# Optimization experiments

Hardware: AMD Instinct MI355X
Metric: run time of the kernel (lower is better)

## Reference

```python
import jax, jax.numpy as jnp
import numpy as np

B, CQ, CKV, H, W = 8, 128, 64, 64, 64
DIM = CQ // 8  # qk_reduction=8 -> 16


def conv1x1(x, w, b):
    # x: [B, Cin, H, W], w: [Cout, Cin], b: [Cout]
    return jnp.einsum('bchw,oc->bohw', x, w) + b[None, :, None, None]


def setup_inputs() -> dict:
    key = jax.random.key(0)
    ks = jax.random.split(key, 12)
    s = 0.05
    return {
        'x4q': jax.random.normal(ks[0], (B, CQ, H, W), jnp.float32),
        'x4kv': jax.random.normal(ks[1], (B, CKV, H, W), jnp.float32),
        'Wq': jax.random.normal(ks[2], (DIM, CQ), jnp.float32) * s,
        'bq': jax.random.normal(ks[3], (DIM,), jnp.float32) * s,
        'Wk': jax.random.normal(ks[4], (DIM, CKV), jnp.float32) * s,
        'bk': jax.random.normal(ks[5], (DIM,), jnp.float32) * s,
        'Wv': jax.random.normal(ks[6], (CQ, CKV), jnp.float32) * s,
        'bv': jax.random.normal(ks[7], (CQ,), jnp.float32) * s,
        'Wo': jax.random.normal(ks[8], (CQ, CQ), jnp.float32) * s,
        'bo': jax.random.normal(ks[9], (CQ,), jnp.float32) * s,
        'gamma': jax.random.normal(ks[10], (1,), jnp.float32) * s,
    }


def reference(x4q, x4kv, Wq, bq, Wk, bk, Wv, bv, Wo, bo, gamma):
    q = conv1x1(x4q, Wq, bq)    # [B, DIM, H, W]
    k = conv1x1(x4kv, Wk, bk)   # [B, DIM, H, W]
    v = conv1x1(x4kv, Wv, bv)   # [B, CQ,  H, W]
    b, dim, h_, w_ = q.shape
    n = h_ * w_
    qf = q.reshape(b, dim, n)
    kf = k.reshape(b, dim, n)
    vf = v.reshape(b, -1, n)
    # score[b, n_query, m_key] = q^T k, scaled by dim^-0.5
    score = jnp.einsum('bdn,bdm->bnm', qf, kf) * (float(dim) ** -0.5)
    attention = jax.nn.softmax(score, axis=2)          # over keys m
    hmat = jnp.einsum('bcm,bnm->bcn', vf, attention)   # bmm(v, att^T)
    hmap = hmat.reshape(b, -1, h_, w_)
    hmap = conv1x1(hmap, Wo, bo)
    return gamma * hmap + x4q
```

## Files before the change

### kernel.cpp

```cpp
#include <hip/hip_runtime.h>

#define NB 8
#define CQ 128
#define CKV 64
#define NPIX 4096
#define QDIM 16
#define KVBLK 128
#define NTI (NPIX / KVBLK)

typedef float f32x4 __attribute__((ext_vector_type(4)));
typedef float f32x16 __attribute__((ext_vector_type(16)));
typedef __bf16 bf16x8 __attribute__((ext_vector_type(8)));
typedef unsigned short u16;
typedef u16 u16x4 __attribute__((ext_vector_type(4)));
typedef u16 u16x8 __attribute__((ext_vector_type(8)));
typedef unsigned int u32;
typedef u32 u32x2 __attribute__((ext_vector_type(2)));
typedef u32 u32x4 __attribute__((ext_vector_type(4)));

static __device__ __forceinline__ u16 f2bf(float f) {
  unsigned int u = __builtin_bit_cast(unsigned int, f);
  u = (u + 0x7FFFu + ((u >> 16) & 1u)) >> 16;
  return (u16)u;
}
static __device__ __forceinline__ u32 cvtpk(float lo, float hi) {
  u32 r; asm("v_cvt_pk_bf16_f32 %0, %1, %2" : "=v"(r) : "v"(lo), "v"(hi)); return r;
}
static __device__ __forceinline__ void plswap(u32& a, u32& b) {
#if __has_builtin(__builtin_amdgcn_permlane32_swap)
  u32x2 r = __builtin_amdgcn_permlane32_swap(a, b, false, false);
  a = r[0]; b = r[1];
#else
  asm volatile("v_permlane32_swap_b32 %0, %1" : "+v"(a), "+v"(b));
#endif
}
static __device__ __forceinline__ void gload_lds16(const void* g, void* l) {
  __builtin_amdgcn_global_load_lds((const __attribute__((address_space(1))) void*)g,
                                   (__attribute__((address_space(3))) void*)l, 16, 0, 0);
}

__global__ __launch_bounds__(256) void proj_qk(
    const float* __restrict__ xq, const float* __restrict__ Wq, const float* __restrict__ bq,
    const float* __restrict__ xkv, const float* __restrict__ Wk, const float* __restrict__ bk,
    u16* __restrict__ Qs, u16* __restrict__ Ks)
{
  __shared__ float wq[QDIM][CQ];
  __shared__ float wk[QDIM][CKV];
  __shared__ float redq[4][64][17];
  __shared__ float redk[4][64][17];
  int t = threadIdx.x;
  for (int i = t; i < QDIM * CQ; i += 256) wq[i >> 7][i & 127] = Wq[i];
  for (int i = t; i < QDIM * CKV; i += 256) wk[i >> 6][i & 63] = Wk[i];
  __syncthreads();
  int b = (int)blockIdx.x >> 6;
  int n0 = ((int)blockIdx.x & 63) << 6;
  int px = t & 63, cg = t >> 6;
  int n = n0 + px;
  const float* xqp = xq + (size_t)b * CQ * NPIX + n;
  const float* xkp = xkv + (size_t)b * CKV * NPIX + n;
  float qa[QDIM], ka[QDIM];
  #pragma unroll
  for (int d = 0; d < QDIM; d++) { qa[d] = 0.f; ka[d] = 0.f; }
  int cq0 = cg * 32, ck0 = cg * 16;
  #pragma unroll 4
  for (int c = cq0; c < cq0 + 32; c++) {
    float x = xqp[(size_t)c * NPIX];
    #pragma unroll
    for (int d = 0; d < QDIM; d++) qa[d] = fmaf(wq[d][c], x, qa[d]);
  }
  #pragma unroll 4
  for (int c = ck0; c < ck0 + 16; c++) {
    float x = xkp[(size_t)c * NPIX];
    #pragma unroll
    for (int d = 0; d < QDIM; d++) ka[d] = fmaf(wk[d][c], x, ka[d]);
  }
  #pragma unroll
  for (int d = 0; d < QDIM; d++) { redq[cg][px][d] = qa[d]; redk[cg][px][d] = ka[d]; }
  __syncthreads();
  const float SC = 0.25f * 1.44269504088896340736f;
  int d0 = cg * 4;
  u16x4 oq, ok;
  #pragma unroll
  for (int j = 0; j < 4; j++) {
    float sq = redq[0][px][d0 + j] + redq[1][px][d0 + j]
             + redq[2][px][d0 + j] + redq[3][px][d0 + j] + bq[d0 + j];
    oq[j] = f2bf(sq * SC);
    float sk = redk[0][px][d0 + j] + redk[1][px][d0 + j]
             + redk[2][px][d0 + j] + redk[3][px][d0 + j] + bk[d0 + j];
    ok[j] = f2bf(sk);
  }
  size_t o = ((size_t)b * NPIX + n) * QDIM + d0;
  *(u16x4*)(Qs + o) = oq;
  *(u16x4*)(Ks + o) = ok;
}

__global__ __launch_bounds__(256) void proj_v(
    const float* __restrict__ xkv, const float* __restrict__ Wv, const float* __restrict__ bv,
    u16* __restrict__ Vt)
{
  __shared__ float wv[CQ][CKV + 1];
  __shared__ float xs[CKV][64 + 4];
  int t = threadIdx.x;
  int b = (int)blockIdx.x >> 6;
  int n0 = ((int)blockIdx.x & 63) << 6;
  for (int i = t; i < CQ * CKV; i += 256) wv[i >> 6][i & 63] = Wv[i];
  const float* xp = xkv + (size_t)b * CKV * NPIX + n0;
  for (int i = t; i < CKV * 16; i += 256) {
    int c = i >> 4, c4 = (i & 15) * 4;
    *(f32x4*)(&xs[c][c4]) = *(const f32x4*)(xp + (size_t)c * NPIX + c4);
  }
  __syncthreads();
  int cog = t >> 4, pg = t & 15;
  int co0 = cog * 8, p0 = pg * 4;
  float acc[8][4];
  #pragma unroll
  for (int j = 0; j < 8; j++) {
    float bb = bv[co0 + j];
    #pragma unroll
    for (int p = 0; p < 4; p++) acc[j][p] = bb;
  }
  #pragma unroll 2
  for (int c = 0; c < CKV; c++) {
    float xv[4];
    #pragma unroll
    for (int p = 0; p < 4; p++) xv[p] = xs[c][p0 + p];
    #pragma unroll
    for (int j = 0; j < 8; j++) {
      float wvv = wv[co0 + j][c];
      #pragma unroll
      for (int p = 0; p < 4; p++) acc[j][p] = fmaf(wvv, xv[p], acc[j][p]);
    }
  }
  #pragma unroll
  for (int j = 0; j < 8; j++) {
    u16x4 ov;
    #pragma unroll
    for (int p = 0; p < 4; p++) ov[p] = f2bf(acc[j][p]);
    *(u16x4*)(Vt + ((size_t)b * CQ + co0 + j) * NPIX + n0 + p0) = ov;
  }
}

__global__ __launch_bounds__(256, 2) void attn(
    const u16* __restrict__ Qs, const u16* __restrict__ Ks, const u16* __restrict__ Vt,
    u16* __restrict__ O)
{
  __shared__ u16 v_s[2][128][128];
  __shared__ float d_red[2][2][32];
  __shared__ float d_inv[2][32];

  int t = (int)threadIdx.x;
  int w = t >> 6, l = t & 63, l31 = l & 31, hi = l >> 5;
  int ph = w;
  int sw = ((int)blockIdx.x & 7) * 64 + ((int)blockIdx.x >> 3);
  int b = sw >> 6, q0 = (sw & 63) * 64;

  const u16* Qb = Qs + (size_t)b * NPIX * QDIM;
  const u16* Kb = Ks + (size_t)b * NPIX * QDIM;
  const u16* Vb = Vt + (size_t)b * CQ * NPIX;

  bf16x8 qf0 = *(const bf16x8*)(Qb + (size_t)(q0 + l31) * QDIM + hi * 8);
  bf16x8 qf1 = *(const bf16x8*)(Qb + (size_t)(q0 + 32 + l31) * QDIM + hi * 8);

  int row0 = w * 32 + (l >> 4);
  int lx = (l & 15) ^ (l >> 4);
  const u16* kp = Kb + (size_t)(ph * 32 + l31) * QDIM + hi * 8;
  int rsw = l31 & 15;

  f32x16 acc0[4], acc1[4];
  #pragma unroll
  for (int cb = 0; cb < 4; cb++)
    #pragma unroll
    for (int r = 0; r < 16; r++) { acc0[cb][r] = 0.f; acc1[cb][r] = 0.f; }
  float lsum0 = 0.f, lsum1 = 0.f;

  u32x4 afw0[2], afw1[2];

  auto PACK = [&](const f32x16& s, u32x4* aw, float& ls) {
    float pv[16];
    #pragma unroll
    for (int r = 0; r < 16; r++) {
      pv[r] = __builtin_amdgcn_exp2f(s[r]);
      ls += pv[r];
    }
    u32 a0 = cvtpk(pv[0], pv[1]),  b0 = cvtpk(pv[2], pv[3]);
    u32 c0 = cvtpk(pv[4], pv[5]),  d0 = cvtpk(pv[6], pv[7]);
    plswap(a0, c0); plswap(b0, d0);
    aw[0] = u32x4{a0, b0, c0, d0};
    u32 a1 = cvtpk(pv[8], pv[9]),  b1 = cvtpk(pv[10], pv[11]);
    u32 c1 = cvtpk(pv[12], pv[13]), d1 = cvtpk(pv[14], pv[15]);
    plswap(a1, c1); plswap(b1, d1);
    aw[1] = u32x4{a1, b1, c1, d1};
  };

  f32x16 z;
  #pragma unroll
  for (int r = 0; r < 16; r++) z[r] = 0.f;

  #pragma unroll
  for (int j = 0; j < 8; j++)
    gload_lds16(Vb + (size_t)(row0 + j * 4) * NPIX + (lx ^ ((j & 3) << 2)) * 8,
                &v_s[0][w * 32 + j * 4][0]);
  bf16x8 kc = *(const bf16x8*)(kp);
  bf16x8 kn = *(const bf16x8*)(kp + (size_t)KVBLK * QDIM);

  #pragma unroll 1
  for (int it = 0; it < NTI; it++) {
    __syncthreads();

    if (it + 1 < NTI) {
      #pragma unroll
      for (int j = 0; j < 8; j++)
        gload_lds16(Vb + (size_t)(row0 + j * 4) * NPIX + (lx ^ ((j & 3) << 2)) * 8
                       + (size_t)(it + 1) * KVBLK,
                    &v_s[(it + 1) & 1][w * 32 + j * 4][0]);
    }

    f32x16 s0 = __builtin_amdgcn_mfma_f32_32x32x16_bf16(kc, qf0, z, 0, 0, 0);
    f32x16 s1 = __builtin_amdgcn_mfma_f32_32x32x16_bf16(kc, qf1, z, 0, 0, 0);
    kc = kn;
    if (it + 2 < NTI) kn = *(const bf16x8*)(kp + (size_t)(it + 2) * KVBLK * QDIM);
    PACK(s0, afw0, lsum0);
    PACK(s1, afw1, lsum1);

    const u16 (*vs)[128] = v_s[it & 1];
    #pragma unroll
    for (int c = 0; c < 2; c++) {
      bf16x8 af0 = __builtin_bit_cast(bf16x8, afw0[c]);
      bf16x8 af1 = __builtin_bit_cast(bf16x8, afw1[c]);
      #pragma unroll
      for (int cb = 0; cb < 4; cb++) {
        int chunk = (ph * 4 + c * 2 + hi) ^ rsw;
        bf16x8 vf = *(const bf16x8*)(&vs[cb * 32 + l31][chunk * 8]);
        acc0[cb] = __builtin_amdgcn_mfma_f32_32x32x16_bf16(af0, vf, acc0[cb], 0, 0, 0);
        acc1[cb] = __builtin_amdgcn_mfma_f32_32x32x16_bf16(af1, vf, acc1[cb], 0, 0, 0);
      }
    }
  }

  float tot0 = lsum0 + __shfl_xor(lsum0, 32);
  float tot1 = lsum1 + __shfl_xor(lsum1, 32);
  __syncthreads();
  float* red = (float*)v_s;
  if (ph >= 2) {
    if (hi == 0) { d_red[ph - 2][0][l31] = tot0; d_red[ph - 2][1][l31] = tot1; }
    float* dst = red + (size_t)(ph - 2) * 64 * 128;
    #pragma unroll
    for (int cb = 0; cb < 4; cb++)
      #pragma unroll
      for (int r = 0; r < 16; r++) {
        int row = (r & 3) + 8 * (r >> 2) + 4 * hi;
        dst[(size_t)row * 128 + cb * 32 + l31] = acc0[cb][r];
        dst[(size_t)(row + 32) * 128 + cb * 32 + l31] = acc1[cb][r];
      }
  }
  __syncthreads();
  if (ph < 2) {
    tot0 += d_red[ph][0][l31];
    tot1 += d_red[ph][1][l31];
    const float* src = red + (size_t)ph * 64 * 128;
    #pragma unroll
    for (int cb = 0; cb < 4; cb++)
      #pragma unroll
      for (int r = 0; r < 16; r++) {
        int row = (r & 3) + 8 * (r >> 2) + 4 * hi;
        acc0[cb][r] += src[(size_t)row * 128 + cb * 32 + l31];
        acc1[cb][r] += src[(size_t)(row + 32) * 128 + cb * 32 + l31];
      }
  }
  __syncthreads();
  if (ph == 1) {
    if (hi == 0) { d_red[0][0][l31] = tot0; d_red[0][1][l31] = tot1; }
    float* dst = red;
    #pragma unroll
    for (int cb = 0; cb < 4; cb++)
      #pragma unroll
      for (int r = 0; r < 16; r++) {
        int row = (r & 3) + 8 * (r >> 2) + 4 * hi;
        dst[(size_t)row * 128 + cb * 32 + l31] = acc0[cb][r];
        dst[(size_t)(row + 32) * 128 + cb * 32 + l31] = acc1[cb][r];
      }
  }
  __syncthreads();
  if (ph == 0) {
    tot0 += d_red[0][0][l31];
    tot1 += d_red[0][1][l31];
    if (hi == 0) { d_inv[0][l31] = 1.0f / tot0; d_inv[1][l31] = 1.0f / tot1; }
    const float* src = red;
    u16* Ob = O + ((size_t)b * NPIX + q0) * CQ;
    #pragma unroll
    for (int cb = 0; cb < 4; cb++)
      #pragma unroll
      for (int r = 0; r < 16; r++) {
        int row = (r & 3) + 8 * (r >> 2) + 4 * hi;
        float v0 = acc0[cb][r] + src[(size_t)row * 128 + cb * 32 + l31];
        float v1 = acc1[cb][r] + src[(size_t)(row + 32) * 128 + cb * 32 + l31];
        Ob[(size_t)row * CQ + cb * 32 + l31] = f2bf(v0 * d_inv[0][row]);
        Ob[(size_t)(row + 32) * CQ + cb * 32 + l31] = f2bf(v1 * d_inv[1][row]);
      }
  }
}

__global__ __launch_bounds__(256) void proj_o(
    const u16* __restrict__ O, const float* __restrict__ Wo, const float* __restrict__ bo,
    const float* __restrict__ gamma, const float* __restrict__ xq, float* __restrict__ out)
{
  __shared__ u16 wo_s[128][136];
  __shared__ float bos[128];
  int t = (int)threadIdx.x, w = t >> 6, l = t & 63, l31 = l & 31, hi = l >> 5;
  int bb = (int)blockIdx.x >> 6;
  int n0 = ((int)blockIdx.x & 63) * 64;
  for (int i = t; i < 128 * 32; i += 256) {
    int r = i >> 5, c4 = (i & 31) * 4;
    f32x4 v = *(const f32x4*)(Wo + r * 128 + c4);
    #pragma unroll
    for (int j = 0; j < 4; j++) wo_s[r][c4 + j] = f2bf(v[j]);
  }
  if (t < 128) bos[t] = bo[t];
  __syncthreads();
  int nw = n0 + (w & 1) * 32;
  int coh = (w >> 1) * 64;
  const u16* Ob = O + ((size_t)bb * NPIX + nw) * CQ;
  f32x16 acc[2];
  #pragma unroll
  for (int cb = 0; cb < 2; cb++)
    #pragma unroll
    for (int r = 0; r < 16; r++) acc[cb][r] = 0.f;
  #pragma unroll
  for (int c = 0; c < 8; c++) {
    bf16x8 of = *(const bf16x8*)(Ob + (size_t)l31 * CQ + c * 16 + hi * 8);
    #pragma unroll
    for (int cb = 0; cb < 2; cb++) {
      bf16x8 wf = *(const bf16x8*)(&wo_s[coh + cb * 32 + l31][c * 16 + hi * 8]);
      acc[cb] = __builtin_amdgcn_mfma_f32_32x32x16_bf16(wf, of, acc[cb], 0, 0, 0);
    }
  }
  float g = gamma[0];
  #pragma unroll
  for (int cb = 0; cb < 2; cb++) {
    #pragma unroll
    for (int r = 0; r < 16; r++) {
      int co = coh + cb * 32 + (r & 3) + 8 * (r >> 2) + 4 * hi;
      size_t idx = ((size_t)bb * CQ + co) * NPIX + nw + l31;
      out[idx] = g * (acc[cb][r] + bos[co]) + xq[idx];
    }
  }
}

extern "C" void kernel_launch(void* const* d_in, const int* in_sizes, int n_in,
                              void* d_out, int out_size, void* d_ws, size_t ws_size,
                              hipStream_t stream) {
  const float* x4q  = (const float*)d_in[0];
  const float* x4kv = (const float*)d_in[1];
  const float* Wq   = (const float*)d_in[2];
  const float* bq   = (const float*)d_in[3];
  const float* Wk   = (const float*)d_in[4];
  const float* bk   = (const float*)d_in[5];
  const float* Wv   = (const float*)d_in[6];
  const float* bv   = (const float*)d_in[7];
  const float* Wo   = (const float*)d_in[8];
  const float* bo   = (const float*)d_in[9];
  const float* gamma = (const float*)d_in[10];
  float* out = (float*)d_out;

  u16* Qs = (u16*)d_ws;
  u16* Ks = Qs + (size_t)NB * NPIX * QDIM;
  u16* Vt = Ks + (size_t)NB * NPIX * QDIM;
  u16* O  = Vt + (size_t)NB * CQ * NPIX;

  proj_qk<<<dim3(NB * 64), dim3(256), 0, stream>>>(x4q, Wq, bq, x4kv, Wk, bk, Qs, Ks);
  proj_v<<<dim3(NB * 64), dim3(256), 0, stream>>>(x4kv, Wv, bv, Vt);
  attn<<<dim3(NB * 64), dim3(256), 0, stream>>>(Qs, Ks, Vt, O);
  proj_o<<<dim3(NB * 64), dim3(256), 0, stream>>>(O, Wo, bo, gamma, x4q, out);
}
```

Measured before the change: 86.11 us.

## Fuse output projection and residual epilogue into attention kernel

Removes the separate proj_o kernel. After the softmax-weighted V accumulation, the attention block normalises its 64-query tile, writes it as bf16 into a swizzled LDS buffer, and multiplies by Wo fragments held in registers using MFMA. It then adds bias, applies gamma and the residual, and writes the final output directly. It also restructures the cross-wave reduction so two waves each finish half the rows, instead of funnelling everything into wave 0. This avoids the global round-trip of the intermediate O tensor and one launch, at the cost of extra registers (woF), per-block Wo reloads, and a longer epilogue inside a kernel with occupancy 2.

```diff
diff --git a/kernel.cpp b/kernel.cpp
--- a/kernel.cpp
+++ b/kernel.cpp
@@ -142,11 +142,15 @@
 
 __global__ __launch_bounds__(256, 2) void attn(
     const u16* __restrict__ Qs, const u16* __restrict__ Ks, const u16* __restrict__ Vt,
-    u16* __restrict__ O)
+    const float* __restrict__ Wo, const float* __restrict__ bo,
+    const float* __restrict__ gamma, const float* __restrict__ xq,
+    float* __restrict__ out)
 {
   __shared__ u16 v_s[2][128][128];
   __shared__ float d_red[2][2][32];
+  __shared__ float d_x[2][32];
   __shared__ float d_inv[2][32];
+  __shared__ float bos[128];
 
   int t = (int)threadIdx.x;
   int w = t >> 6, l = t & 63, l31 = l & 31, hi = l >> 5;
@@ -157,6 +161,8 @@
   const u16* Qb = Qs + (size_t)b * NPIX * QDIM;
   const u16* Kb = Ks + (size_t)b * NPIX * QDIM;
   const u16* Vb = Vt + (size_t)b * CQ * NPIX;
+
+  if (t < 128) bos[t] = bo[t];
 
   bf16x8 qf0 = *(const bf16x8*)(Qb + (size_t)(q0 + l31) * QDIM + hi * 8);
   bf16x8 qf1 = *(const bf16x8*)(Qb + (size_t)(q0 + 32 + l31) * QDIM + hi * 8);
@@ -239,6 +245,20 @@
 
   float tot0 = lsum0 + __shfl_xor(lsum0, 32);
   float tot1 = lsum1 + __shfl_xor(lsum1, 32);
+
+  bf16x8 woF[8];
+  {
+    const float* wrow = Wo + (size_t)(w * 32 + l31) * CQ + hi * 8;
+    #pragma unroll
+    for (int kc8 = 0; kc8 < 8; kc8++) {
+      f32x4 a = *(const f32x4*)(wrow + kc8 * 16);
+      f32x4 c4 = *(const f32x4*)(wrow + kc8 * 16 + 4);
+      u32x4 pk = { cvtpk(a[0], a[1]), cvtpk(a[2], a[3]),
+                   cvtpk(c4[0], c4[1]), cvtpk(c4[2], c4[3]) };
+      woF[kc8] = __builtin_bit_cast(bf16x8, pk);
+    }
+  }
+
   __syncthreads();
   float* red = (float*)v_s;
   if (ph >= 2) {
@@ -266,82 +286,90 @@
         acc0[cb][r] += src[(size_t)row * 128 + cb * 32 + l31];
         acc1[cb][r] += src[(size_t)(row + 32) * 128 + cb * 32 + l31];
       }
-  }
-  __syncthreads();
-  if (ph == 1) {
-    if (hi == 0) { d_red[0][0][l31] = tot0; d_red[0][1][l31] = tot1; }
-    float* dst = red;
+    if (ph == 0) {
+      if (hi == 0) d_x[0][l31] = tot1;
+      #pragma unroll
+      for (int cb = 0; cb < 4; cb++)
+        #pragma unroll
+        for (int r = 0; r < 16; r++) {
+          int row = (r & 3) + 8 * (r >> 2) + 4 * hi;
+          red[(size_t)(row + 32) * 128 + cb * 32 + l31] = acc1[cb][r];
+        }
+    } else {
+      if (hi == 0) d_x[1][l31] = tot0;
+      #pragma unroll
+      for (int cb = 0; cb < 4; cb++)
+        #pragma unroll
+        for (int r = 0; r < 16; r++) {
+          int row = (r & 3) + 8 * (r >> 2) + 4 * hi;
+          red[8192 + (size_t)row * 128 + cb * 32 + l31] = acc0[cb][r];
+        }
+    }
+  }
+  __syncthreads();
+  if (ph == 0) {
+    float denom = tot0 + d_x[1][l31];
+    if (hi == 0) d_inv[0][l31] = 1.0f / denom;
     #pragma unroll
     for (int cb = 0; cb < 4; cb++)
       #pragma unroll
       for (int r = 0; r < 16; r++) {
         int row = (r & 3) + 8 * (r >> 2) + 4 * hi;
-        dst[(size_t)row * 128 + cb * 32 + l31] = acc0[cb][r];
-        dst[(size_t)(row + 32) * 128 + cb * 32 + l31] = acc1[cb][r];
-      }
-  }
-  __syncthreads();
+        acc0[cb][r] += red[8192 + (size_t)row * 128 + cb * 32 + l31];
+      }
+  } else if (ph == 1) {
+    float denom = tot1 + d_x[0][l31];
+    if (hi == 0) d_inv[1][l31] = 1.0f / denom;
+    #pragma unroll
+    for (int cb = 0; cb < 4; cb++)
+      #pragma unroll
+      for (int r = 0; r < 16; r++) {
+        int row = (r & 3) + 8 * (r >> 2) + 4 * hi;
+        acc1[cb][r] += red[(size_t)(row + 32) * 128 + cb * 32 + l31];
+      }
+  }
+  __syncthreads();
+  u16* Old = (u16*)v_s;
   if (ph == 0) {
-    tot0 += d_red[0][0][l31];
-    tot1 += d_red[0][1][l31];
-    if (hi == 0) { d_inv[0][l31] = 1.0f / tot0; d_inv[1][l31] = 1.0f / tot1; }
-    const float* src = red;
-    u16* Ob = O + ((size_t)b * NPIX + q0) * CQ;
     #pragma unroll
     for (int cb = 0; cb < 4; cb++)
       #pragma unroll
       for (int r = 0; r < 16; r++) {
         int row = (r & 3) + 8 * (r >> 2) + 4 * hi;
-        float v0 = acc0[cb][r] + src[(size_t)row * 128 + cb * 32 + l31];
-        float v1 = acc1[cb][r] + src[(size_t)(row + 32) * 128 + cb * 32 + l31];
-        Ob[(size_t)row * CQ + cb * 32 + l31] = f2bf(v0 * d_inv[0][row]);
-        Ob[(size_t)(row + 32) * CQ + cb * 32 + l31] = f2bf(v1 * d_inv[1][row]);
-      }
-  }
-}
-
-__global__ __launch_bounds__(256) void proj_o(
-    const u16* __restrict__ O, const float* __restrict__ Wo, const float* __restrict__ bo,
-    const float* __restrict__ gamma, const float* __restrict__ xq, float* __restrict__ out)
-{
-  __shared__ u16 wo_s[128][136];
-  __shared__ float bos[128];
-  int t = (int)threadIdx.x, w = t >> 6, l = t & 63, l31 = l & 31, hi = l >> 5;
-  int bb = (int)blockIdx.x >> 6;
-  int n0 = ((int)blockIdx.x & 63) * 64;
-  for (int i = t; i < 128 * 32; i += 256) {
-    int r = i >> 5, c4 = (i & 31) * 4;
-    f32x4 v = *(const f32x4*)(Wo + r * 128 + c4);
-    #pragma unroll
-    for (int j = 0; j < 4; j++) wo_s[r][c4 + j] = f2bf(v[j]);
-  }
-  if (t < 128) bos[t] = bo[t];
-  __syncthreads();
-  int nw = n0 + (w & 1) * 32;
-  int coh = (w >> 1) * 64;
-  const u16* Ob = O + ((size_t)bb * NPIX + nw) * CQ;
-  f32x16 acc[2];
-  #pragma unroll
-  for (int cb = 0; cb < 2; cb++)
-    #pragma unroll
-    for (int r = 0; r < 16; r++) acc[cb][r] = 0.f;
-  #pragma unroll
-  for (int c = 0; c < 8; c++) {
-    bf16x8 of = *(const bf16x8*)(Ob + (size_t)l31 * CQ + c * 16 + hi * 8);
-    #pragma unroll
-    for (int cb = 0; cb < 2; cb++) {
-      bf16x8 wf = *(const bf16x8*)(&wo_s[coh + cb * 32 + l31][c * 16 + hi * 8]);
-      acc[cb] = __builtin_amdgcn_mfma_f32_32x32x16_bf16(wf, of, acc[cb], 0, 0, 0);
-    }
-  }
+        int c = cb * 32 + l31;
+        Old[row * 128 + (((c >> 3) ^ (row & 15)) << 3) + (c & 7)] =
+            f2bf(acc0[cb][r] * d_inv[0][row]);
+      }
+  } else if (ph == 1) {
+    #pragma unroll
+    for (int cb = 0; cb < 4; cb++)
+      #pragma unroll
+      for (int r = 0; r < 16; r++) {
+        int q = 32 + (r & 3) + 8 * (r >> 2) + 4 * hi;
+        int c = cb * 32 + l31;
+        Old[q * 128 + (((c >> 3) ^ (q & 15)) << 3) + (c & 7)] =
+            f2bf(acc1[cb][r] * d_inv[1][(q - 32)]);
+      }
+  }
+  __syncthreads();
   float g = gamma[0];
-  #pragma unroll
-  for (int cb = 0; cb < 2; cb++) {
+  const float* xb = xq + (size_t)b * CQ * NPIX;
+  float* ob = out + (size_t)b * CQ * NPIX;
+  #pragma unroll
+  for (int qb = 0; qb < 2; qb++) {
+    f32x16 e = z;
+    int q = qb * 32 + l31;
+    #pragma unroll
+    for (int kc8 = 0; kc8 < 8; kc8++) {
+      int phys = (kc8 * 2 + hi) ^ (l31 & 15);
+      bf16x8 of = *(const bf16x8*)(Old + q * 128 + phys * 8);
+      e = __builtin_amdgcn_mfma_f32_32x32x16_bf16(woF[kc8], of, e, 0, 0, 0);
+    }
     #pragma unroll
     for (int r = 0; r < 16; r++) {
-      int co = coh + cb * 32 + (r & 3) + 8 * (r >> 2) + 4 * hi;
-      size_t idx = ((size_t)bb * CQ + co) * NPIX + nw + l31;
-      out[idx] = g * (acc[cb][r] + bos[co]) + xq[idx];
+      int o = w * 32 + (r & 3) + 8 * (r >> 2) + 4 * hi;
+      size_t idx = (size_t)o * NPIX + q0 + qb * 32 + l31;
+      ob[idx] = g * (e[r] + bos[o]) + xb[idx];
     }
   }
 }
@@ -365,10 +393,8 @@
   u16* Qs = (u16*)d_ws;
   u16* Ks = Qs + (size_t)NB * NPIX * QDIM;
   u16* Vt = Ks + (size_t)NB * NPIX * QDIM;
-  u16* O  = Vt + (size_t)NB * CQ * NPIX;
 
   proj_qk<<<dim3(NB * 64), dim3(256), 0, stream>>>(x4q, Wq, bq, x4kv, Wk, bk, Qs, Ks);
   proj_v<<<dim3(NB * 64), dim3(256), 0, stream>>>(x4kv, Wv, bv, Vt);
-  attn<<<dim3(NB * 64), dim3(256), 0, stream>>>(Qs, Ks, Vt, O);
-  proj_o<<<dim3(NB * 64), dim3(256), 0, stream>>>(O, Wo, bo, gamma, x4q, out);
-}
+  attn<<<dim3(NB * 64), dim3(256), 0, stream>>>(Qs, Ks, Vt, Wo, bo, gamma, x4q, out);
+}
```

Measured after the change: 84.41 us. 1.02x faster.
